# Kernel tuning notes

Hardware: AMD Instinct MI355X
Metric: run time of the kernel (lower is better)

The kernel has to match this reference:

```python
import jax, jax.numpy as jnp
import numpy as np

N_NODES = 100000
N_EDGES = 1600000
NFEAT, NHID, NCLASS = 512, 256, 128
K_HOPS = 5
ALPHA = 0.1


def setup_inputs() -> dict:
    key = jax.random.key(0)
    ks = jax.random.split(key, 7)
    x = jax.random.normal(ks[0], (N_NODES, NFEAT), dtype=jnp.float32)
    edge_index = jax.random.randint(ks[1], (2, N_EDGES), 0, N_NODES, dtype=jnp.int64)
    edge_weight = jax.random.uniform(ks[2], (N_EDGES,), dtype=jnp.float32)
    # Glorot-ish scaled linear weights
    W1 = jax.random.normal(ks[3], (NFEAT, NHID), dtype=jnp.float32) * (1.0 / np.sqrt(NFEAT))
    b1 = jnp.zeros((NHID,), dtype=jnp.float32)
    W2 = jax.random.normal(ks[4], (NHID, NCLASS), dtype=jnp.float32) * (1.0 / np.sqrt(NHID))
    b2 = jnp.zeros((NCLASS,), dtype=jnp.float32)
    return {"x": x, "edge_index": edge_index, "edge_weight": edge_weight,
            "W1": W1, "b1": b1, "W2": W2, "b2": b2}


def reference(x, edge_index, edge_weight, W1, b1, W2, b2):
    # 2-layer MLP (act after first layer only; dropout p=0)
    h = jnp.maximum(x @ W1 + b1, 0.0)
    h = h @ W2 + b2  # [N, nclass]
    src = edge_index[0]
    dst = edge_index[1]
    x0 = h

    def step(carry, _):
        # gather by source, scale by edge weight, scatter-add at target
        msg = carry[src] * edge_weight[:, None]          # [E, nclass]
        agg = jax.ops.segment_sum(msg, dst, num_segments=N_NODES)
        out = (1.0 - ALPHA) * agg + ALPHA * x0           # restart mix
        return out, None

    xK, _ = jax.lax.scan(step, x0, None, length=K_HOPS)
    return jax.nn.log_softmax(xK, axis=1)
```

## Files before the change

kernel.cpp:

```cpp
#include <hip/hip_runtime.h>
#include <hip/hip_bf16.h>
#include <cstdint>
#include <cstddef>

#define N_NODES 100000
#define NFEAT 512
#define NHID 256
#define NCLASS 128
#define K_HOPS 5
#define ALPHA 0.1f

typedef __attribute__((ext_vector_type(8))) short short8v;
typedef __attribute__((ext_vector_type(4))) float f32x4;

__device__ __forceinline__ unsigned short f2bf(float f) {
    unsigned u = __builtin_bit_cast(unsigned, f);
    u += 0x7FFFu + ((u >> 16) & 1u);
    return (unsigned short)(u >> 16);
}
__device__ __forceinline__ float bflo(unsigned u) {
    return __builtin_bit_cast(float, u << 16);
}
__device__ __forceinline__ float bfhi(unsigned u) {
    return __builtin_bit_cast(float, u & 0xFFFF0000u);
}
__device__ __forceinline__ unsigned cvtpk2(float a, float b) {
    unsigned r;
    asm("v_cvt_pk_bf16_f32 %0, %1, %2" : "=v"(r) : "v"(a), "v"(b));
    return r;
}


__global__ void count_kernel(const int* __restrict__ dst, int* __restrict__ counts, int E) {
    int i = blockIdx.x * blockDim.x + threadIdx.x;
    if (i < E) atomicAdd(&counts[dst[i]], 1);
}

__global__ __launch_bounds__(256) void scan_p1(const int* __restrict__ counts,
                                               int* __restrict__ partial, int n) {
    __shared__ int ws[4];
    int b = blockIdx.x, t = threadIdx.x;
    int base = b * 1024 + t * 4;
    int s = 0;
#pragma unroll
    for (int j = 0; j < 4; ++j) {
        int idx = base + j;
        if (idx < n) s += counts[idx];
    }
#pragma unroll
    for (int off = 32; off; off >>= 1) s += __shfl_xor(s, off, 64);
    if ((t & 63) == 0) ws[t >> 6] = s;
    __syncthreads();
    if (t == 0) partial[b] = ws[0] + ws[1] + ws[2] + ws[3];
}

__global__ __launch_bounds__(128) void scan_p2(int* __restrict__ partial, int nb) {
    __shared__ int s[128];
    int t = threadIdx.x;
    int v = (t < nb) ? partial[t] : 0;
    s[t] = v;
    __syncthreads();
    for (int off = 1; off < 128; off <<= 1) {
        int u = (t >= off) ? s[t - off] : 0;
        __syncthreads();
        s[t] += u;
        __syncthreads();
    }
    if (t < nb) partial[t] = (t == 0) ? 0 : s[t - 1];
}

__global__ __launch_bounds__(256) void scan_p3(const int* __restrict__ counts,
                                               const int* __restrict__ partial,
                                               int* __restrict__ row_ptr,
                                               int* __restrict__ fill, int n) {
    __shared__ int ts[256];
    int b = blockIdx.x, t = threadIdx.x;
    int base = b * 1024 + t * 4;
    int c[4];
#pragma unroll
    for (int j = 0; j < 4; ++j) {
        int idx = base + j;
        c[j] = (idx < n) ? counts[idx] : 0;
    }
    int s = c[0] + c[1] + c[2] + c[3];
    ts[t] = s;
    __syncthreads();
    for (int off = 1; off < 256; off <<= 1) {
        int v = (t >= off) ? ts[t - off] : 0;
        __syncthreads();
        ts[t] += v;
        __syncthreads();
    }
    int pre = partial[b] + ((t == 0) ? 0 : ts[t - 1]);
#pragma unroll
    for (int j = 0; j < 4; ++j) {
        int idx = base + j;
        if (idx < n) {
            row_ptr[idx] = pre;
            fill[idx] = pre;
            if (idx == n - 1) row_ptr[n] = pre + c[j];
            pre += c[j];
        }
    }
}

__global__ void scatter_kernel(const int* __restrict__ src, const int* __restrict__ dst,
                               const float* __restrict__ w, int* __restrict__ fill,
                               int2* __restrict__ epk, int E) {
    int i = blockIdx.x * blockDim.x + threadIdx.x;
    if (i < E) {
        int d = dst[i];
        int pos = atomicAdd(&fill[d], 1);
        int2 m; m.x = src[i]; m.y = __builtin_bit_cast(int, w[i]);
        epk[pos] = m;
    }
}

__global__ void wtrans_kernel(const float* __restrict__ W, unsigned short* __restrict__ Wt,
                              int K, int N) {
    int idx = blockIdx.x * blockDim.x + threadIdx.x;
    if (idx >= N * K) return;
    int n = idx / K, k = idx - n * K;
    Wt[idx] = f2bf(W[(size_t)k * N + n]);
}

template<int K, int N, int RELU, int AF32>
__global__ __launch_bounds__(256) void gemm_mfma(const void* __restrict__ Ain,
                                                 const unsigned short* __restrict__ Wt,
                                                 const float* __restrict__ bias,
                                                 unsigned short* __restrict__ Cout, int M) {
    __shared__ unsigned short As[4096];
    __shared__ unsigned short Bs[4096];
    const int tid = threadIdx.x;
    const int lane = tid & 63;
    const int wv = tid >> 6;
    const int wr = wv >> 1, wc = wv & 1;
    const int brow = blockIdx.y * 128;
    const int bcol = blockIdx.x * 128;
    const float* Af = (const float*)Ain;
    const unsigned short* Ab = (const unsigned short*)Ain;

    int arow[2], browb[2], kc[2];
#pragma unroll
    for (int i = 0; i < 2; ++i) {
        int g = tid + i * 256, l6 = g & 63;
        int r = (g >> 6) * 16 + (l6 & 15);
        kc[i] = (l6 >> 4) * 8;
        int ra = brow + r; if (ra > M - 1) ra = M - 1;
        arow[i] = ra;
        browb[i] = bcol + r;
    }

    f32x4 acc[4][4];
#pragma unroll
    for (int m = 0; m < 4; ++m)
#pragma unroll
        for (int n = 0; n < 4; ++n) acc[m][n] = f32x4{0.f, 0.f, 0.f, 0.f};

    float4 pa0[2], pa1[2];
    short8v pab[2];
    short8v pb[2];

#pragma unroll
    for (int i = 0; i < 2; ++i) {
        if constexpr (AF32) {
            const float* s = &Af[(size_t)arow[i] * K + kc[i]];
            pa0[i] = *(const float4*)s;
            pa1[i] = *(const float4*)(s + 4);
        } else {
            pab[i] = *(const short8v*)&Ab[(size_t)arow[i] * K + kc[i]];
        }
        pb[i] = *(const short8v*)&Wt[(size_t)browb[i] * K + kc[i]];
    }

    for (int k0 = 0; k0 < K; k0 += 32) {
#pragma unroll
        for (int i = 0; i < 2; ++i) {
            int g = tid + i * 256;
            if constexpr (AF32) {
                uint4 u;
                u.x = cvtpk2(pa0[i].x, pa0[i].y);
                u.y = cvtpk2(pa0[i].z, pa0[i].w);
                u.z = cvtpk2(pa1[i].x, pa1[i].y);
                u.w = cvtpk2(pa1[i].z, pa1[i].w);
                *(uint4*)&As[g * 8] = u;
            } else {
                *(short8v*)&As[g * 8] = pab[i];
            }
            *(short8v*)&Bs[g * 8] = pb[i];
        }
        __syncthreads();
        if (k0 + 32 < K) {
#pragma unroll
            for (int i = 0; i < 2; ++i) {
                if constexpr (AF32) {
                    const float* s = &Af[(size_t)arow[i] * K + k0 + 32 + kc[i]];
                    pa0[i] = *(const float4*)s;
                    pa1[i] = *(const float4*)(s + 4);
                } else {
                    pab[i] = *(const short8v*)&Ab[(size_t)arow[i] * K + k0 + 32 + kc[i]];
                }
                pb[i] = *(const short8v*)&Wt[(size_t)browb[i] * K + k0 + 32 + kc[i]];
            }
        }
        short8v a[4], b[4];
#pragma unroll
        for (int m = 0; m < 4; ++m)
            a[m] = *(const short8v*)&As[((wr * 4 + m) * 64 + lane) * 8];
#pragma unroll
        for (int n = 0; n < 4; ++n)
            b[n] = *(const short8v*)&Bs[((wc * 4 + n) * 64 + lane) * 8];
#pragma unroll
        for (int m = 0; m < 4; ++m)
#pragma unroll
            for (int n = 0; n < 4; ++n)
                acc[m][n] = __builtin_amdgcn_mfma_f32_16x16x32_bf16(a[m], b[n], acc[m][n], 0, 0, 0);
        __syncthreads();
    }

#pragma unroll
    for (int n = 0; n < 4; ++n) {
        int colg = bcol + wc * 64 + n * 16 + (lane & 15);
        float bv = bias[colg];
#pragma unroll
        for (int m = 0; m < 4; ++m) {
#pragma unroll
            for (int r = 0; r < 4; ++r) {
                int rowg = brow + wr * 64 + m * 16 + (lane >> 4) * 4 + r;
                if (rowg < M) {
                    float v = acc[m][n][r] + bv;
                    if constexpr (RELU) v = fmaxf(v, 0.f);
                    Cout[(size_t)rowg * N + colg] = f2bf(v);
                }
            }
        }
    }
}

template<int FINAL>
__global__ __launch_bounds__(256) void hop_kernel(const unsigned short* __restrict__ carry,
                                                  const unsigned short* __restrict__ c0,
                                                  const int* __restrict__ rp,
                                                  const int2* __restrict__ epk,
                                                  unsigned short* __restrict__ outb,
                                                  float* __restrict__ outf, int nnodes) {
    int node = blockIdx.x * 4 + (threadIdx.x >> 6);
    if (node >= nnodes) return;
    int lane = threadIdx.x & 63;
    int e0 = rp[node], e1 = rp[node + 1];

    float a0x = 0.f, a0y = 0.f, a1x = 0.f, a1y = 0.f;
    float a2x = 0.f, a2y = 0.f, a3x = 0.f, a3y = 0.f;

    for (int eb = e0; eb < e1; eb += 64) {
        int nb = e1 - eb; if (nb > 64) nb = 64;
        int cs = 0, wvi = 0;
        if (lane < nb) {
            int2 m = epk[eb + lane];
            cs = m.x; wvi = m.y;
        }
        int j = 0;
        for (; j + 7 < nb; j += 8) {
            int s0 = __builtin_amdgcn_readlane(cs, j);
            int s1 = __builtin_amdgcn_readlane(cs, j + 1);
            int s2 = __builtin_amdgcn_readlane(cs, j + 2);
            int s3 = __builtin_amdgcn_readlane(cs, j + 3);
            int s4 = __builtin_amdgcn_readlane(cs, j + 4);
            int s5 = __builtin_amdgcn_readlane(cs, j + 5);
            int s6 = __builtin_amdgcn_readlane(cs, j + 6);
            int s7 = __builtin_amdgcn_readlane(cs, j + 7);
            float w0 = __builtin_bit_cast(float, __builtin_amdgcn_readlane(wvi, j));
            float w1 = __builtin_bit_cast(float, __builtin_amdgcn_readlane(wvi, j + 1));
            float w2 = __builtin_bit_cast(float, __builtin_amdgcn_readlane(wvi, j + 2));
            float w3 = __builtin_bit_cast(float, __builtin_amdgcn_readlane(wvi, j + 3));
            float w4 = __builtin_bit_cast(float, __builtin_amdgcn_readlane(wvi, j + 4));
            float w5 = __builtin_bit_cast(float, __builtin_amdgcn_readlane(wvi, j + 5));
            float w6 = __builtin_bit_cast(float, __builtin_amdgcn_readlane(wvi, j + 6));
            float w7 = __builtin_bit_cast(float, __builtin_amdgcn_readlane(wvi, j + 7));
            unsigned u0 = ((const unsigned*)(carry + ((size_t)s0 << 7)))[lane];
            unsigned u1 = ((const unsigned*)(carry + ((size_t)s1 << 7)))[lane];
            unsigned u2 = ((const unsigned*)(carry + ((size_t)s2 << 7)))[lane];
            unsigned u3 = ((const unsigned*)(carry + ((size_t)s3 << 7)))[lane];
            unsigned u4 = ((const unsigned*)(carry + ((size_t)s4 << 7)))[lane];
            unsigned u5 = ((const unsigned*)(carry + ((size_t)s5 << 7)))[lane];
            unsigned u6 = ((const unsigned*)(carry + ((size_t)s6 << 7)))[lane];
            unsigned u7 = ((const unsigned*)(carry + ((size_t)s7 << 7)))[lane];
            a0x = fmaf(w0, bflo(u0), a0x); a0y = fmaf(w0, bfhi(u0), a0y);
            a1x = fmaf(w1, bflo(u1), a1x); a1y = fmaf(w1, bfhi(u1), a1y);
            a2x = fmaf(w2, bflo(u2), a2x); a2y = fmaf(w2, bfhi(u2), a2y);
            a3x = fmaf(w3, bflo(u3), a3x); a3y = fmaf(w3, bfhi(u3), a3y);
            a0x = fmaf(w4, bflo(u4), a0x); a0y = fmaf(w4, bfhi(u4), a0y);
            a1x = fmaf(w5, bflo(u5), a1x); a1y = fmaf(w5, bfhi(u5), a1y);
            a2x = fmaf(w6, bflo(u6), a2x); a2y = fmaf(w6, bfhi(u6), a2y);
            a3x = fmaf(w7, bflo(u7), a3x); a3y = fmaf(w7, bfhi(u7), a3y);
        }
        for (; j + 3 < nb; j += 4) {
            int s0 = __builtin_amdgcn_readlane(cs, j);
            int s1 = __builtin_amdgcn_readlane(cs, j + 1);
            int s2 = __builtin_amdgcn_readlane(cs, j + 2);
            int s3 = __builtin_amdgcn_readlane(cs, j + 3);
            float w0 = __builtin_bit_cast(float, __builtin_amdgcn_readlane(wvi, j));
            float w1 = __builtin_bit_cast(float, __builtin_amdgcn_readlane(wvi, j + 1));
            float w2 = __builtin_bit_cast(float, __builtin_amdgcn_readlane(wvi, j + 2));
            float w3 = __builtin_bit_cast(float, __builtin_amdgcn_readlane(wvi, j + 3));
            unsigned u0 = ((const unsigned*)(carry + ((size_t)s0 << 7)))[lane];
            unsigned u1 = ((const unsigned*)(carry + ((size_t)s1 << 7)))[lane];
            unsigned u2 = ((const unsigned*)(carry + ((size_t)s2 << 7)))[lane];
            unsigned u3 = ((const unsigned*)(carry + ((size_t)s3 << 7)))[lane];
            a0x = fmaf(w0, bflo(u0), a0x); a0y = fmaf(w0, bfhi(u0), a0y);
            a1x = fmaf(w1, bflo(u1), a1x); a1y = fmaf(w1, bfhi(u1), a1y);
            a2x = fmaf(w2, bflo(u2), a2x); a2y = fmaf(w2, bfhi(u2), a2y);
            a3x = fmaf(w3, bflo(u3), a3x); a3y = fmaf(w3, bfhi(u3), a3y);
        }
        for (; j < nb; ++j) {
            int s0 = __builtin_amdgcn_readlane(cs, j);
            float w0 = __builtin_bit_cast(float, __builtin_amdgcn_readlane(wvi, j));
            unsigned u0 = ((const unsigned*)(carry + ((size_t)s0 << 7)))[lane];
            a0x = fmaf(w0, bflo(u0), a0x); a0y = fmaf(w0, bfhi(u0), a0y);
        }
    }

    unsigned ux = ((const unsigned*)(c0 + ((size_t)node << 7)))[lane];
    float vx = (1.f - ALPHA) * (a0x + a1x + a2x + a3x) + ALPHA * bflo(ux);
    float vy = (1.f - ALPHA) * (a0y + a1y + a2y + a3y) + ALPHA * bfhi(ux);

    if (FINAL) {
        float mx = fmaxf(vx, vy);
#pragma unroll
        for (int off = 32; off; off >>= 1) mx = fmaxf(mx, __shfl_xor(mx, off, 64));
        float se = __expf(vx - mx) + __expf(vy - mx);
#pragma unroll
        for (int off = 32; off; off >>= 1) se += __shfl_xor(se, off, 64);
        float l = mx + __logf(se);
        float2 o; o.x = vx - l; o.y = vy - l;
        ((float2*)(outf + ((size_t)node << 7)))[lane] = o;
    } else {
        unsigned o = (unsigned)f2bf(vx) | ((unsigned)f2bf(vy) << 16);
        ((unsigned*)(outb + ((size_t)node << 7)))[lane] = o;
    }
}


extern "C" void kernel_launch(void* const* d_in, const int* in_sizes, int n_in,
                              void* d_out, int out_size, void* d_ws, size_t ws_size,
                              hipStream_t stream) {
    const float* x   = (const float*)d_in[0];
    const int*   ei  = (const int*)d_in[1];
    const float* ew  = (const float*)d_in[2];
    const float* W1  = (const float*)d_in[3];
    const float* b1  = (const float*)d_in[4];
    const float* W2  = (const float*)d_in[5];
    const float* b2  = (const float*)d_in[6];
    float* outp = (float*)d_out;

    const int E = in_sizes[1] / 2;
    const int Nn = N_NODES;
    const int* srcv = ei;
    const int* dstv = ei + E;
    const size_t NC = (size_t)Nn * NCLASS;

    unsigned short* c0  = (unsigned short*)d_ws;
    unsigned short* A16 = c0 + NC;
    unsigned short* B16 = A16 + NC;
    unsigned short* hb  = A16;
    unsigned short* w1t = B16 + NC;
    unsigned short* w2t = w1t + NHID * NFEAT;
    int* row_ptr = (int*)(w2t + NCLASS * NHID);
    int* fill    = row_ptr + (Nn + 1);
    int* partial = fill + Nn;
    int2* epk    = (int2*)(partial + 128);

    const int NB = (Nn + 1023) / 1024;

    hipMemsetAsync(fill, 0, (size_t)Nn * sizeof(int), stream);
    count_kernel<<<(E + 255) / 256, 256, 0, stream>>>(dstv, fill, E);
    scan_p1<<<NB, 256, 0, stream>>>(fill, partial, Nn);
    scan_p2<<<1, 128, 0, stream>>>(partial, NB);
    scan_p3<<<NB, 256, 0, stream>>>(fill, partial, row_ptr, fill, Nn);
    scatter_kernel<<<(E + 255) / 256, 256, 0, stream>>>(srcv, dstv, ew, fill, epk, E);

    wtrans_kernel<<<(NHID * NFEAT + 255) / 256, 256, 0, stream>>>(W1, w1t, NFEAT, NHID);
    wtrans_kernel<<<(NCLASS * NHID + 255) / 256, 256, 0, stream>>>(W2, w2t, NHID, NCLASS);

    {
        dim3 g1(NHID / 128, (Nn + 127) / 128);
        gemm_mfma<NFEAT, NHID, 1, 1><<<g1, 256, 0, stream>>>(x, w1t, b1, hb, Nn);
        dim3 g2(NCLASS / 128, (Nn + 127) / 128);
        gemm_mfma<NHID, NCLASS, 0, 0><<<g2, 256, 0, stream>>>(hb, w2t, b2, c0, Nn);
    }

    int grid = (Nn + 3) / 4;
    const unsigned short* carry = c0;
    unsigned short* dsts[2] = {A16, B16};
    for (int k = 0; k < K_HOPS - 1; ++k) {
        unsigned short* o = dsts[k & 1];
        hop_kernel<0><<<grid, 256, 0, stream>>>(carry, c0, row_ptr, epk, o, nullptr, Nn);
        carry = o;
    }
    hop_kernel<1><<<grid, 256, 0, stream>>>(carry, c0, row_ptr, epk, nullptr, outp, Nn);
}
```

Baseline: 684.6 us.

## Use direct global-to-LDS loads with double-buffered LDS in MFMA GEMM

Replaces the register-staged GEMM tile loads with global_load_lds DMA-style loads into double-buffered shared memory, prefetching the next K-step while computing the current one. For the fp32 input GEMM, the bf16 conversion moves from before the LDS store to after the LDS read, so LDS holds fp32 tiles and LDS usage grows to 48KB. This aims to cut register pressure and VGPR round trips and to overlap loads with MFMA. The cost is more LDS per block, which may lower occupancy, plus a full vmcnt wait every step.

```diff
diff --git a/kernel.cpp b/kernel.cpp
--- a/kernel.cpp
+++ b/kernel.cpp
@@ -28,6 +28,10 @@
     unsigned r;
     asm("v_cvt_pk_bf16_f32 %0, %1, %2" : "=v"(r) : "v"(a), "v"(b));
     return r;
+}
+__device__ __forceinline__ void gload_lds16(const void* g, void* l) {
+    __builtin_amdgcn_global_load_lds((const __attribute__((address_space(1))) void*)g,
+                                     (__attribute__((address_space(3))) void*)l, 16, 0, 0);
 }
 
 
@@ -129,8 +133,13 @@
                                                  const unsigned short* __restrict__ Wt,
                                                  const float* __restrict__ bias,
                                                  unsigned short* __restrict__ Cout, int M) {
-    __shared__ unsigned short As[4096];
-    __shared__ unsigned short Bs[4096];
+    extern __shared__ char smem[];
+    constexpr int ABYTES = AF32 ? 16384 : 8192;
+    constexpr int ASTEP  = AF32 ? 128 : 64;
+    constexpr int NCA    = AF32 ? 4 : 2;
+    char* Abase = smem;
+    char* Bbase = smem + 2 * ABYTES;
+
     const int tid = threadIdx.x;
     const int lane = tid & 63;
     const int wv = tid >> 6;
@@ -140,15 +149,24 @@
     const float* Af = (const float*)Ain;
     const unsigned short* Ab = (const unsigned short*)Ain;
 
-    int arow[2], browb[2], kc[2];
-#pragma unroll
-    for (int i = 0; i < 2; ++i) {
-        int g = tid + i * 256, l6 = g & 63;
-        int r = (g >> 6) * 16 + (l6 & 15);
-        kc[i] = (l6 >> 4) * 8;
-        int ra = brow + r; if (ra > M - 1) ra = M - 1;
-        arow[i] = ra;
-        browb[i] = bcol + r;
+    const char* asrc[NCA];
+    int aci[NCA];
+#pragma unroll
+    for (int c = 0; c < NCA; ++c) {
+        int ci = wv + c * 4;
+        aci[c] = ci;
+        int ms = AF32 ? (ci & 7) : ci;
+        int koff = (lane >> 4) * 8 + (AF32 ? (ci >> 3) * 4 : 0);
+        int ar = brow + ms * 16 + (lane & 15); if (ar > M - 1) ar = M - 1;
+        asrc[c] = AF32 ? (const char*)&Af[(size_t)ar * K + koff]
+                       : (const char*)&Ab[(size_t)ar * K + koff];
+    }
+    const char* bsrc[2];
+#pragma unroll
+    for (int c = 0; c < 2; ++c) {
+        int ci = wv + c * 4;
+        int bc = bcol + ci * 16 + (lane & 15);
+        bsrc[c] = (const char*)&Wt[(size_t)bc * K + (lane >> 4) * 8];
     }
 
     f32x4 acc[4][4];
@@ -157,65 +175,59 @@
 #pragma unroll
         for (int n = 0; n < 4; ++n) acc[m][n] = f32x4{0.f, 0.f, 0.f, 0.f};
 
-    float4 pa0[2], pa1[2];
-    short8v pab[2];
-    short8v pb[2];
-
-#pragma unroll
-    for (int i = 0; i < 2; ++i) {
+    auto stage = [&](int buf, int step) {
+        char* la = Abase + buf * ABYTES;
+        char* lb = Bbase + buf * 8192;
+#pragma unroll
+        for (int c = 0; c < NCA; ++c)
+            gload_lds16(asrc[c] + (size_t)step * ASTEP, la + aci[c] * 1024);
+#pragma unroll
+        for (int c = 0; c < 2; ++c)
+            gload_lds16(bsrc[c] + (size_t)step * 64, lb + (wv + c * 4) * 1024);
+    };
+
+    constexpr int NSTEP = K / 32;
+    int cur = 0;
+    stage(0, 0);
+    asm volatile("s_waitcnt vmcnt(0)" ::: "memory");
+    __syncthreads();
+
+    for (int s = 0; s < NSTEP; ++s) {
+        if (s + 1 < NSTEP) stage(cur ^ 1, s + 1);
+
+        short8v a[4], b[4];
         if constexpr (AF32) {
-            const float* s = &Af[(size_t)arow[i] * K + kc[i]];
-            pa0[i] = *(const float4*)s;
-            pa1[i] = *(const float4*)(s + 4);
+            const float* Asf = (const float*)(Abase + cur * ABYTES);
+#pragma unroll
+            for (int m = 0; m < 4; ++m) {
+                int g = (wr * 4 + m) * 64 + lane;
+                f32x4 lo = *(const f32x4*)&Asf[g * 4];
+                f32x4 hi = *(const f32x4*)&Asf[(512 + g) * 4];
+                uint4 u;
+                u.x = cvtpk2(lo[0], lo[1]); u.y = cvtpk2(lo[2], lo[3]);
+                u.z = cvtpk2(hi[0], hi[1]); u.w = cvtpk2(hi[2], hi[3]);
+                a[m] = __builtin_bit_cast(short8v, u);
+            }
         } else {
-            pab[i] = *(const short8v*)&Ab[(size_t)arow[i] * K + kc[i]];
-        }
-        pb[i] = *(const short8v*)&Wt[(size_t)browb[i] * K + kc[i]];
-    }
-
-    for (int k0 = 0; k0 < K; k0 += 32) {
-#pragma unroll
-        for (int i = 0; i < 2; ++i) {
-            int g = tid + i * 256;
-            if constexpr (AF32) {
-                uint4 u;
-                u.x = cvtpk2(pa0[i].x, pa0[i].y);
-                u.y = cvtpk2(pa0[i].z, pa0[i].w);
-                u.z = cvtpk2(pa1[i].x, pa1[i].y);
-                u.w = cvtpk2(pa1[i].z, pa1[i].w);
-                *(uint4*)&As[g * 8] = u;
-            } else {
-                *(short8v*)&As[g * 8] = pab[i];
-            }
-            *(short8v*)&Bs[g * 8] = pb[i];
-        }
-        __syncthreads();
-        if (k0 + 32 < K) {
-#pragma unroll
-            for (int i = 0; i < 2; ++i) {
-                if constexpr (AF32) {
-                    const float* s = &Af[(size_t)arow[i] * K + k0 + 32 + kc[i]];
-                    pa0[i] = *(const float4*)s;
-                    pa1[i] = *(const float4*)(s + 4);
-                } else {
-                    pab[i] = *(const short8v*)&Ab[(size_t)arow[i] * K + k0 + 32 + kc[i]];
-                }
-                pb[i] = *(const short8v*)&Wt[(size_t)browb[i] * K + k0 + 32 + kc[i]];
-            }
-        }
-        short8v a[4], b[4];
-#pragma unroll
-        for (int m = 0; m < 4; ++m)
-            a[m] = *(const short8v*)&As[((wr * 4 + m) * 64 + lane) * 8];
+            const unsigned short* As16 = (const unsigned short*)(Abase + cur * ABYTES);
+#pragma unroll
+            for (int m = 0; m < 4; ++m)
+                a[m] = *(const short8v*)&As16[((wr * 4 + m) * 64 + lane) * 8];
+        }
+        const unsigned short* Bs16 = (const unsigned short*)(Bbase + cur * 8192);
 #pragma unroll
         for (int n = 0; n < 4; ++n)
-            b[n] = *(const short8v*)&Bs[((wc * 4 + n) * 64 + lane) * 8];
+            b[n] = *(const short8v*)&Bs16[((wc * 4 + n) * 64 + lane) * 8];
+
 #pragma unroll
         for (int m = 0; m < 4; ++m)
 #pragma unroll
             for (int n = 0; n < 4; ++n)
                 acc[m][n] = __builtin_amdgcn_mfma_f32_16x16x32_bf16(a[m], b[n], acc[m][n], 0, 0, 0);
+
+        asm volatile("s_waitcnt vmcnt(0)" ::: "memory");
         __syncthreads();
+        cur ^= 1;
     }
 
 #pragma unroll
@@ -384,9 +396,9 @@
 
     {
         dim3 g1(NHID / 128, (Nn + 127) / 128);
-        gemm_mfma<NFEAT, NHID, 1, 1><<<g1, 256, 0, stream>>>(x, w1t, b1, hb, Nn);
+        gemm_mfma<NFEAT, NHID, 1, 1><<<g1, 256, 49152, stream>>>(x, w1t, b1, hb, Nn);
         dim3 g2(NCLASS / 128, (Nn + 127) / 128);
-        gemm_mfma<NHID, NCLASS, 0, 0><<<g2, 256, 0, stream>>>(hb, w2t, b2, c0, Nn);
+        gemm_mfma<NHID, NCLASS, 0, 0><<<g2, 256, 32768, stream>>>(hb, w2t, b2, c0, Nn);
     }
 
     int grid = (Nn + 3) / 4;
```

Result: faster. 666.6 us (-2.6%).
